# Performance work log

Hardware: AMD Instinct MI355X
Metric: run time of the kernel (lower is better)

## Reference

```python
import jax, jax.numpy as jnp
import numpy as np
import math

D_MODEL = 1024
NUM_HEADS = 16
D_K = D_MODEL // NUM_HEADS
MAX_SEQ_LEN = 2048
ROPE_THETA = 10000.0
BATCH = 4
SEQ = 2048


def _rope_buffers():
    inv_freq = 1.0 / (ROPE_THETA ** (jnp.arange(0, D_K, 2, dtype=jnp.float32) / D_K))
    positions = jnp.arange(MAX_SEQ_LEN, dtype=jnp.float32)
    angles = jnp.einsum('i,j->ij', positions, inv_freq)  # [max_seq_len, d_k/2]
    return jnp.cos(angles), jnp.sin(angles)


def setup_inputs() -> dict:
    key = jax.random.key(0)
    kx, kq, kk, kv, ko = jax.random.split(key, 5)
    std = math.sqrt(2.0 / (D_MODEL + D_MODEL))
    x = jax.random.normal(kx, (BATCH, SEQ, D_MODEL), dtype=jnp.float32)
    pos_ids = jnp.broadcast_to(jnp.arange(SEQ, dtype=jnp.int64), (BATCH, SEQ))
    Wq = jax.random.normal(kq, (D_MODEL, D_MODEL), dtype=jnp.float32) * std
    Wk = jax.random.normal(kk, (D_MODEL, D_MODEL), dtype=jnp.float32) * std
    Wv = jax.random.normal(kv, (D_MODEL, D_MODEL), dtype=jnp.float32) * std
    Wo = jax.random.normal(ko, (D_MODEL, D_MODEL), dtype=jnp.float32) * std
    cos, sin = _rope_buffers()
    return {"x": x, "pos_ids": pos_ids, "Wq": Wq, "Wk": Wk, "Wv": Wv, "Wo": Wo, "cos": cos, "sin": sin}


def _apply_rope(t, pos_ids, cos, sin):
    # t: [B, H, S, D_K]; interleaved (even, odd) pair rotation, as in the torch module
    cp = cos[pos_ids][:, None, :, :]  # [B,1,S,D_K/2]
    sp = sin[pos_ids][:, None, :, :]
    tr = t.reshape(*t.shape[:-1], D_K // 2, 2)
    t0, t1 = tr[..., 0], tr[..., 1]
    rot = jnp.stack((t0 * cp - t1 * sp, t0 * sp + t1 * cp), axis=-1)
    return rot.reshape(t.shape)


def reference(x, pos_ids, Wq, Wk, Wv, Wo, cos, sin):
    B, S, _ = x.shape
    def proj(W):
        return jnp.matmul(x, W.T).reshape(B, S, NUM_HEADS, D_K).transpose(0, 2, 1, 3)
    Q = _apply_rope(proj(Wq), pos_ids, cos, sin)
    K = _apply_rope(proj(Wk), pos_ids, cos, sin)
    V = proj(Wv)
    scores = jnp.einsum('bhqd,bhkd->bhqk', Q, K) / math.sqrt(D_K)
    causal = jnp.tril(jnp.ones((S, S), dtype=bool))
    scores = jnp.where(causal, scores, -jnp.inf)
    attn = jax.nn.softmax(scores, axis=-1)
    out = jnp.einsum('bhqk,bhkd->bhqd', attn, V)
    out = out.transpose(0, 2, 1, 3).reshape(B, S, D_MODEL)
    return jnp.matmul(out, Wo.T)
```

## Files before the change

kernel.cpp:

```cpp
#include <hip/hip_runtime.h>
#include <hip/hip_bf16.h>

typedef __bf16 bf16;
typedef __bf16 bf16x4 __attribute__((ext_vector_type(4)));
typedef __bf16 bf16x8 __attribute__((ext_vector_type(8)));
typedef float f32x4 __attribute__((ext_vector_type(4)));
typedef unsigned int u32;

#define BATCH 4
#define SEQN 2048
#define NH 16
#define DK 64
#define DM 1024
#define MROWS (BATCH*SEQN)

__device__ __forceinline__ void async16(bf16* lds, const bf16* g) {
  __builtin_amdgcn_global_load_lds(
      (const __attribute__((address_space(1))) u32*)g,
      (__attribute__((address_space(3))) u32*)lds, 16, 0, 0);
}

__global__ void cvt_all_kernel(const float4* __restrict__ x,  const float4* __restrict__ wq,
                               const float4* __restrict__ wk, const float4* __restrict__ wv,
                               const float4* __restrict__ wo,
                               bf16x4* __restrict__ xb, bf16x4* __restrict__ wqkvb,
                               bf16x4* __restrict__ wob) {
  const int NX = MROWS*DM/4, NW = DM*DM/4;
  int i = blockIdx.x*256 + threadIdx.x;
  const float4* s; bf16x4* d; int j;
  if (i < NX)             { s = x;  d = xb;         j = i; }
  else if (i < NX+NW)     { s = wq; d = wqkvb;      j = i-NX; }
  else if (i < NX+2*NW)   { s = wk; d = wqkvb+NW;   j = i-NX-NW; }
  else if (i < NX+3*NW)   { s = wv; d = wqkvb+2*NW; j = i-NX-2*NW; }
  else if (i < NX+4*NW)   { s = wo; d = wob;        j = i-NX-3*NW; }
  else return;
  float4 f = s[j];
  bf16x4 v;
  v[0] = (bf16)f.x; v[1] = (bf16)f.y; v[2] = (bf16)f.z; v[3] = (bf16)f.w;
  d[j] = v;
}

__device__ __forceinline__ void stage_half(bf16* slot, const bf16* src) {
  const int tid = threadIdx.x; const int w = tid >> 6;
#pragma unroll
  for (int j = 0; j < 2; ++j) {
    int L = j*512 + tid;
    int row = L >> 3;
    int dc  = (L & 7) ^ (row & 7);
    async16(slot + (size_t)(j*512 + w*64)*8, src + (size_t)row*DM + dc*8);
  }
}

#define SBAR() do { __builtin_amdgcn_sched_barrier(0); \
                    __builtin_amdgcn_s_barrier();       \
                    __builtin_amdgcn_sched_barrier(0); } while(0)

#define GPHASE(Ab, Bb, Q, STAGE, FW)  do {                                       \
    bf16x8 afr[2][2];                                                            \
    _Pragma("unroll")                                                            \
    for (int m = 0; m < 2; ++m) {                                                \
      const int row = wm + ((2*(Q)+m)<<4) + lc;                                  \
      _Pragma("unroll")                                                          \
      for (int kk = 0; kk < 2; ++kk)                                             \
        afr[m][kk] = *(const bf16x8*)((Ab) + (size_t)((row<<3) + ((kk*4+quad) ^ (row&7)))*8); \
    }                                                                            \
    if ((Q) == 0) {                                                              \
      _Pragma("unroll")                                                          \
      for (int nt = 0; nt < 4; ++nt) {                                           \
        const int row = wn + (nt<<4) + lc;                                       \
        _Pragma("unroll")                                                        \
        for (int kk = 0; kk < 2; ++kk)                                           \
          bfr[nt][kk] = *(const bf16x8*)((Bb) + (size_t)((row<<3) + ((kk*4+quad) ^ (row&7)))*8); \
      }                                                                          \
    }                                                                            \
    STAGE;                                                                       \
    SBAR();                                                                      \
    asm volatile("s_waitcnt lgkmcnt(0)" ::: "memory");                           \
    __builtin_amdgcn_sched_barrier(0);                                           \
    __builtin_amdgcn_s_setprio(1);                                               \
    _Pragma("unroll")                                                            \
    for (int kk = 0; kk < 2; ++kk)                                               \
      _Pragma("unroll")                                                          \
      for (int m = 0; m < 2; ++m)                                                \
        _Pragma("unroll")                                                        \
        for (int nt = 0; nt < 4; ++nt)                                           \
          acc[2*(Q)+m][nt] = __builtin_amdgcn_mfma_f32_16x16x32_bf16(afr[m][kk], bfr[nt][kk], acc[2*(Q)+m][nt], 0, 0, 0); \
    __builtin_amdgcn_s_setprio(0);                                               \
    FW;                                                                          \
    SBAR();                                                                      \
  } while (0)

__device__ __forceinline__ void gemm_core256(const bf16* __restrict__ Ag,
    const bf16* __restrict__ Bg, int r0, int c0, bf16* sm, f32x4 (&acc)[8][4]) {
  const int tid  = threadIdx.x;
  const int lane = tid & 63, quad = lane >> 4, lc = lane & 15;
  const int w = tid >> 6;
  const int wm = (w >> 2)*128, wn = (w & 3)*64;
  const int NT = DM/64;
  bf16* As[2] = { sm,         sm + 16384 };
  bf16* Bs[2] = { sm + 32768, sm + 49152 };

  auto stA = [&](int t, int h) {
    int tt = t < NT ? t : NT-1;
    stage_half(As[t&1] + h*8192, Ag + (size_t)(r0 + h*128)*DM + tt*64);
  };
  auto stB = [&](int t, int h) {
    int tt = t < NT ? t : NT-1;
    stage_half(Bs[t&1] + h*8192, Bg + (size_t)(c0 + h*128)*DM + tt*64);
  };

  stA(0,0); stA(0,1); stB(0,0); stB(0,1);
  stB(1,0); stB(1,1);
  asm volatile("s_waitcnt vmcnt(4)" ::: "memory");
  SBAR();

  bf16x8 bfr[4][2];
  for (int X = 0; X < NT/2; ++X) {
    const int t0 = 2*X;
    GPHASE(As[0], Bs[0], 0, stA(t0+1,0), );
    GPHASE(As[0], Bs[0], 1, stA(t0+1,1), );
    GPHASE(As[0], Bs[0], 2, stB(t0+2,0), );
    GPHASE(As[0], Bs[0], 3, stB(t0+2,1), asm volatile("s_waitcnt vmcnt(4)" ::: "memory"));
    GPHASE(As[1], Bs[1], 0, stA(t0+2,0), );
    GPHASE(As[1], Bs[1], 1, stA(t0+2,1), );
    GPHASE(As[1], Bs[1], 2, stB(t0+3,0), );
    GPHASE(As[1], Bs[1], 3, stB(t0+3,1), asm volatile("s_waitcnt vmcnt(4)" ::: "memory"));
  }
}

#define VS 136
__global__ __launch_bounds__(512, 2) void gemm_qkv_kernel(const bf16* __restrict__ A,
    const bf16* __restrict__ Bt, const float* __restrict__ cosb, const float* __restrict__ sinb,
    bf16* __restrict__ Q, bf16* __restrict__ K, bf16* __restrict__ Vt) {
  __shared__ __align__(16) bf16 sm[65536];
  f32x4 acc[8][4] = {};
  const int r0 = blockIdx.y*256, c0 = blockIdx.x*256;
  gemm_core256(A, Bt, r0, c0, sm, acc);
  const int tid  = threadIdx.x;
  const int lane = tid & 63, quad = lane >> 4, lc = lane & 15;
  const int w = tid >> 6;
  const int wm = (w >> 2)*128, wn = (w & 3)*64;
  const int which = c0 >> 10;
  if (which < 2) {
    bf16* T = which == 0 ? Q : K;
#pragma unroll
    for (int mt = 0; mt < 8; ++mt)
#pragma unroll
      for (int r = 0; r < 4; ++r) {
        int gr = r0 + wm + mt*16 + quad*4 + r;
        int b = gr >> 11, s = gr & (SEQN-1);
#pragma unroll
        for (int nt = 0; nt < 4; ++nt) {
          int gc = c0 + wn + nt*16 + lc;
          int c = gc & (DM-1), h = c >> 6, d = c & 63, p = d >> 1;
          float cc = cosb[s*32 + p], ss = sinb[s*32 + p];
          float v  = acc[mt][nt][r];
          float ov = __shfl_xor(v, 1, 64);
          float outv = ((lc & 1) == 0) ? (v*cc - ov*ss) : (ov*ss + v*cc);
          T[(((size_t)(b*NH + h))*SEQN + s)*DK + d] = (bf16)outv;
        }
      }
  } else {
    asm volatile("s_waitcnt vmcnt(0)" ::: "memory");
    __builtin_amdgcn_sched_barrier(0);
    __syncthreads();
    const int b = r0 >> 11, s_base = r0 & (SEQN-1);
    const int h0 = (c0 & (DM-1)) >> 6;
#pragma unroll
    for (int p = 0; p < 2; ++p) {
      if ((w >> 2) == p) {
#pragma unroll
        for (int mt = 0; mt < 8; ++mt)
#pragma unroll
          for (int nt = 0; nt < 4; ++nt) {
            int col = wn + nt*16 + lc;
            bf16x4 vv;
#pragma unroll
            for (int r = 0; r < 4; ++r) vv[r] = (bf16)acc[mt][nt][r];
            *(bf16x4*)(sm + (size_t)col*VS + mt*16 + quad*4) = vv;
          }
      }
      __syncthreads();
#pragma unroll
      for (int it = 0; it < 8; ++it) {
        int dall = it*32 + (tid >> 4);
        int s_off = (tid & 15)*8;
        bf16x8 vv = *(const bf16x8*)(sm + (size_t)dall*VS + s_off);
        int h = h0 + (dall >> 6), d = dall & 63;
        *(bf16x8*)(Vt + (((size_t)(b*NH + h))*DK + d)*SEQN + s_base + p*128 + s_off) = vv;
      }
      __syncthreads();
    }
  }
}

__global__ __launch_bounds__(512, 2) void gemm_out_kernel(const bf16* __restrict__ A,
    const bf16* __restrict__ Bt, float* __restrict__ C) {
  __shared__ __align__(16) bf16 sm[65536];
  f32x4 acc[8][4] = {};
  const int r0 = blockIdx.y*256, c0 = blockIdx.x*256;
  gemm_core256(A, Bt, r0, c0, sm, acc);
  const int tid  = threadIdx.x;
  const int lane = tid & 63, quad = lane >> 4, lc = lane & 15;
  const int w = tid >> 6;
  const int wm = (w >> 2)*128, wn = (w & 3)*64;
#pragma unroll
  for (int mt = 0; mt < 8; ++mt)
#pragma unroll
    for (int nt = 0; nt < 4; ++nt)
#pragma unroll
      for (int r = 0; r < 4; ++r) {
        int gr = r0 + wm + mt*16 + quad*4 + r;
        int gc = c0 + wn + nt*16 + lc;
        C[(size_t)gr*DM + gc] = acc[mt][nt][r];
      }
}

__global__ __launch_bounds__(256, 3) void attn_kernel(const bf16* __restrict__ Q,
    const bf16* __restrict__ K, const bf16* __restrict__ Vt, bf16* __restrict__ Oa) {
  __shared__ __align__(16) bf16 Ks[2][64*64];
  __shared__ __align__(16) bf16 Vs[2][64*64];
  __shared__ __align__(16) bf16 Pw[4][32*72];
  const int tid  = threadIdx.x;
  const int w = tid >> 6, lane = tid & 63;
  const int quad = lane >> 4, lc = lane & 15;
  const int bh = blockIdx.x;
  const int qt = (SEQN/128 - 1) - blockIdx.y;
  const int q0 = qt*128;
  const int qr0 = q0 + w*32;
  const bf16* Qp = Q  + (size_t)bh*SEQN*DK;
  const bf16* Kp = K  + (size_t)bh*SEQN*DK;
  const bf16* Vp = Vt + (size_t)bh*DK*SEQN;
  const float SC = 0.125f * 1.44269504f;
  bf16x8 aq[2][2];
#pragma unroll
  for (int mt = 0; mt < 2; ++mt)
#pragma unroll
    for (int kk = 0; kk < 2; ++kk) {
      bf16x8 raw = *(const bf16x8*)(Qp + (size_t)(qr0 + mt*16 + lc)*DK + kk*32 + quad*8);
#pragma unroll
      for (int j = 0; j < 8; ++j) raw[j] = (bf16)((float)raw[j] * SC);
      aq[mt][kk] = raw;
    }
  f32x4 o[2][4] = {};
  float lrow[2][4] = {};
  bf16* P = Pw[w];
  const int nsteps = 2*(qt + 1);

  auto stage = [&](int kt, int buf) {
#pragma unroll
    for (int j = 0; j < 2; ++j) {
      int L = j*256 + w*64 + lane;
      int row = L >> 3;
      int s8  = (L & 7) ^ (row & 7);
      bf16* kb = &Ks[buf][(size_t)(j*256 + w*64)*8];
      async16(kb, Kp + (size_t)(kt*64 + row)*DK + s8*8);
      bf16* vb = &Vs[buf][(size_t)(j*256 + w*64)*8];
      async16(vb, Vp + (size_t)row*SEQN + kt*64 + s8*8);
    }
  };

  stage(0, 0);
  for (int kt = 0; kt < nsteps; ++kt) {
    const int k0 = kt*64;
    const int cbuf = kt & 1;
    __syncthreads();
    if (kt + 1 < nsteps) stage(kt + 1, cbuf ^ 1);
    if (k0 <= qr0 + 31) {
      const bf16* Kt = Ks[cbuf];
      const bf16* Vc = Vs[cbuf];
      const int lastkey = qr0 + 31;
      f32x4 st[2][4] = {};
#pragma unroll
      for (int kk = 0; kk < 2; ++kk) {
        const int dc = kk*4 + quad;
        bf16x8 bk[4];
#pragma unroll
        for (int nt = 0; nt < 4; ++nt) {
          if (k0 + nt*16 <= lastkey) {
            int kr = nt*16 + lc;
            bk[nt] = *(const bf16x8*)(Kt + (size_t)(kr*8 + (dc ^ (kr & 7)))*8);
          }
        }
#pragma unroll
        for (int nt = 0; nt < 4; ++nt) {
          if (k0 + nt*16 <= lastkey) {
#pragma unroll
            for (int mt = 0; mt < 2; ++mt)
              st[mt][nt] = __builtin_amdgcn_mfma_f32_16x16x32_bf16(aq[mt][kk], bk[nt], st[mt][nt], 0, 0, 0);
          }
        }
      }
#pragma unroll
      for (int mt = 0; mt < 2; ++mt) {
        const int rmin = qr0 + mt*16, rmax = rmin + 15;
#pragma unroll
        for (int nt = 0; nt < 4; ++nt) {
          const int kmin = k0 + nt*16, kmax = kmin + 15;
          f32x4 p;
          if (kmax <= rmin) {
#pragma unroll
            for (int r = 0; r < 4; ++r) p[r] = exp2f(st[mt][nt][r]);
          } else if (kmin > rmax) {
            p = f32x4{0.f, 0.f, 0.f, 0.f};
          } else {
            const int key = kmin + lc;
#pragma unroll
            for (int r = 0; r < 4; ++r) {
              float v = exp2f(st[mt][nt][r]);
              p[r] = (key > rmin + quad*4 + r) ? 0.f : v;
            }
          }
          st[mt][nt] = p;
#pragma unroll
          for (int r = 0; r < 4; ++r) lrow[mt][r] += p[r];
        }
      }
#pragma unroll
      for (int mt = 0; mt < 2; ++mt)
#pragma unroll
        for (int r = 0; r < 4; ++r)
#pragma unroll
          for (int nt = 0; nt < 4; ++nt)
            P[(mt*16 + quad*4 + r)*72 + nt*16 + lc] = (bf16)st[mt][nt][r];
      asm volatile("s_waitcnt lgkmcnt(0)" ::: "memory");
#pragma unroll
      for (int kk = 0; kk < 2; ++kk) {
        if (k0 + kk*32 <= lastkey) {
          bf16x8 ap[2];
#pragma unroll
          for (int mt = 0; mt < 2; ++mt)
            ap[mt] = *(const bf16x8*)(P + (mt*16 + lc)*72 + kk*32 + quad*8);
          const int kc = kk*4 + quad;
          bf16x8 bv[4];
#pragma unroll
          for (int nb = 0; nb < 4; ++nb) {
            int dr = nb*16 + lc;
            bv[nb] = *(const bf16x8*)(Vc + (size_t)(dr*8 + (kc ^ (dr & 7)))*8);
          }
#pragma unroll
          for (int mt = 0; mt < 2; ++mt)
#pragma unroll
            for (int nb = 0; nb < 4; ++nb)
              o[mt][nb] = __builtin_amdgcn_mfma_f32_16x16x32_bf16(ap[mt], bv[nb], o[mt][nb], 0, 0, 0);
        }
      }
      asm volatile("s_waitcnt lgkmcnt(0)" ::: "memory");
    }
  }
#pragma unroll
  for (int off = 1; off < 16; off <<= 1)
#pragma unroll
    for (int mt = 0; mt < 2; ++mt)
#pragma unroll
      for (int r = 0; r < 4; ++r)
        lrow[mt][r] += __shfl_xor(lrow[mt][r], off, 64);
  const int b = bh >> 4, h = bh & 15;
#pragma unroll
  for (int mt = 0; mt < 2; ++mt)
#pragma unroll
    for (int r = 0; r < 4; ++r) {
      float inv = 1.f / lrow[mt][r];
      int qrow = qr0 + mt*16 + quad*4 + r;
      size_t rowoff = ((size_t)b*SEQN + qrow)*DM + h*DK;
#pragma unroll
      for (int nb = 0; nb < 4; ++nb)
        Oa[rowoff + nb*16 + lc] = (bf16)(o[mt][nb][r]*inv);
    }
}

extern "C" void kernel_launch(void* const* d_in, const int* in_sizes, int n_in,
                              void* d_out, int out_size, void* d_ws, size_t ws_size,
                              hipStream_t stream) {
  const float* x    = (const float*)d_in[0];
  const float* Wq   = (const float*)d_in[2];
  const float* Wk   = (const float*)d_in[3];
  const float* Wv   = (const float*)d_in[4];
  const float* Wo   = (const float*)d_in[5];
  const float* cosb = (const float*)d_in[6];
  const float* sinb = (const float*)d_in[7];
  float* out = (float*)d_out;

  char* ws = (char*)d_ws;
  const size_t SZ_X  = (size_t)MROWS*DM*2;
  const size_t SZ_W  = (size_t)DM*DM*2;
  bf16* xb   = (bf16*)(ws);
  bf16* wqkv = (bf16*)(ws + SZ_X);
  bf16* wo_b = (bf16*)(ws + SZ_X + 3*SZ_W);
  bf16* Qb   = (bf16*)(ws + SZ_X + 4*SZ_W);
  bf16* Kb   = (bf16*)(ws + 2*SZ_X + 4*SZ_W);
  bf16* Vtb  = (bf16*)(ws + 3*SZ_X + 4*SZ_W);
  bf16* Oa   = (bf16*)(ws + 4*SZ_X + 4*SZ_W);

  {
    const int NX = MROWS*DM/4, NW = DM*DM/4;
    int nblk = (NX + 4*NW + 255)/256;
    cvt_all_kernel<<<nblk, 256, 0, stream>>>((const float4*)x, (const float4*)Wq,
        (const float4*)Wk, (const float4*)Wv, (const float4*)Wo,
        (bf16x4*)xb, (bf16x4*)wqkv, (bf16x4*)wo_b);
  }
  gemm_qkv_kernel<<<dim3(3*DM/256, MROWS/256), 512, 0, stream>>>(xb, wqkv, cosb, sinb, Qb, Kb, Vtb);
  attn_kernel<<<dim3(BATCH*NH, SEQN/128), 256, 0, stream>>>(Qb, Kb, Vtb, Oa);
  gemm_out_kernel<<<dim3(DM/256, MROWS/256), 512, 0, stream>>>(Oa, wo_b, out);
}
```

Measured before the change: 268.4 us.

## Shrink GEMM tiles to 128x256 and use native exp2 in attention

```diff
diff --git a/kernel.cpp b/kernel.cpp
--- a/kernel.cpp
+++ b/kernel.cpp
@@ -90,26 +90,26 @@
     SBAR();                                                                      \
   } while (0)
 
-__device__ __forceinline__ void gemm_core256(const bf16* __restrict__ Ag,
-    const bf16* __restrict__ Bg, int r0, int c0, bf16* sm, f32x4 (&acc)[8][4]) {
+__device__ __forceinline__ void gemm_core128x256(const bf16* __restrict__ Ag,
+    const bf16* __restrict__ Bg, int r0, int c0, bf16* sm, f32x4 (&acc)[4][4]) {
   const int tid  = threadIdx.x;
   const int lane = tid & 63, quad = lane >> 4, lc = lane & 15;
   const int w = tid >> 6;
-  const int wm = (w >> 2)*128, wn = (w & 3)*64;
+  const int wm = (w >> 2)*64, wn = (w & 3)*64;
   const int NT = DM/64;
-  bf16* As[2] = { sm,         sm + 16384 };
-  bf16* Bs[2] = { sm + 32768, sm + 49152 };
-
-  auto stA = [&](int t, int h) {
+  bf16* As_[2] = { sm,         sm + 8192  };
+  bf16* Bs_[2] = { sm + 16384, sm + 32768 };
+
+  auto stA = [&](int t) {
     int tt = t < NT ? t : NT-1;
-    stage_half(As[t&1] + h*8192, Ag + (size_t)(r0 + h*128)*DM + tt*64);
+    stage_half(As_[t&1], Ag + (size_t)r0*DM + tt*64);
   };
   auto stB = [&](int t, int h) {
     int tt = t < NT ? t : NT-1;
-    stage_half(Bs[t&1] + h*8192, Bg + (size_t)(c0 + h*128)*DM + tt*64);
+    stage_half(Bs_[t&1] + h*8192, Bg + (size_t)(c0 + h*128)*DM + tt*64);
   };
 
-  stA(0,0); stA(0,1); stB(0,0); stB(0,1);
+  stB(0,0); stB(0,1); stA(0);
   stB(1,0); stB(1,1);
   asm volatile("s_waitcnt vmcnt(4)" ::: "memory");
   SBAR();
@@ -117,14 +117,10 @@
   bf16x8 bfr[4][2];
   for (int X = 0; X < NT/2; ++X) {
     const int t0 = 2*X;
-    GPHASE(As[0], Bs[0], 0, stA(t0+1,0), );
-    GPHASE(As[0], Bs[0], 1, stA(t0+1,1), );
-    GPHASE(As[0], Bs[0], 2, stB(t0+2,0), );
-    GPHASE(As[0], Bs[0], 3, stB(t0+2,1), asm volatile("s_waitcnt vmcnt(4)" ::: "memory"));
-    GPHASE(As[1], Bs[1], 0, stA(t0+2,0), );
-    GPHASE(As[1], Bs[1], 1, stA(t0+2,1), );
-    GPHASE(As[1], Bs[1], 2, stB(t0+3,0), );
-    GPHASE(As[1], Bs[1], 3, stB(t0+3,1), asm volatile("s_waitcnt vmcnt(4)" ::: "memory"));
+    GPHASE(As_[0], Bs_[0], 0, stA(t0+1), );
+    GPHASE(As_[0], Bs_[0], 1, stB(t0+2,0); stB(t0+2,1), asm volatile("s_waitcnt vmcnt(4)" ::: "memory"));
+    GPHASE(As_[1], Bs_[1], 0, stA(t0+2), );
+    GPHASE(As_[1], Bs_[1], 1, stB(t0+3,0); stB(t0+3,1), asm volatile("s_waitcnt vmcnt(4)" ::: "memory"));
   }
 }
 
@@ -132,19 +128,19 @@
 __global__ __launch_bounds__(512, 2) void gemm_qkv_kernel(const bf16* __restrict__ A,
     const bf16* __restrict__ Bt, const float* __restrict__ cosb, const float* __restrict__ sinb,
     bf16* __restrict__ Q, bf16* __restrict__ K, bf16* __restrict__ Vt) {
-  __shared__ __align__(16) bf16 sm[65536];
-  f32x4 acc[8][4] = {};
-  const int r0 = blockIdx.y*256, c0 = blockIdx.x*256;
-  gemm_core256(A, Bt, r0, c0, sm, acc);
+  __shared__ __align__(16) bf16 sm[49152];
+  f32x4 acc[4][4] = {};
+  const int r0 = blockIdx.y*128, c0 = blockIdx.x*256;
+  gemm_core128x256(A, Bt, r0, c0, sm, acc);
   const int tid  = threadIdx.x;
   const int lane = tid & 63, quad = lane >> 4, lc = lane & 15;
   const int w = tid >> 6;
-  const int wm = (w >> 2)*128, wn = (w & 3)*64;
+  const int wm = (w >> 2)*64, wn = (w & 3)*64;
   const int which = c0 >> 10;
   if (which < 2) {
     bf16* T = which == 0 ? Q : K;
 #pragma unroll
-    for (int mt = 0; mt < 8; ++mt)
+    for (int mt = 0; mt < 4; ++mt)
 #pragma unroll
       for (int r = 0; r < 4; ++r) {
         int gr = r0 + wm + mt*16 + quad*4 + r;
@@ -164,48 +160,42 @@
     asm volatile("s_waitcnt vmcnt(0)" ::: "memory");
     __builtin_amdgcn_sched_barrier(0);
     __syncthreads();
+#pragma unroll
+    for (int mt = 0; mt < 4; ++mt)
+#pragma unroll
+      for (int nt = 0; nt < 4; ++nt) {
+        int col = wn + nt*16 + lc;
+        bf16x4 vv;
+#pragma unroll
+        for (int r = 0; r < 4; ++r) vv[r] = (bf16)acc[mt][nt][r];
+        *(bf16x4*)(sm + (size_t)col*VS + wm + mt*16 + quad*4) = vv;
+      }
+    __syncthreads();
     const int b = r0 >> 11, s_base = r0 & (SEQN-1);
     const int h0 = (c0 & (DM-1)) >> 6;
 #pragma unroll
-    for (int p = 0; p < 2; ++p) {
-      if ((w >> 2) == p) {
-#pragma unroll
-        for (int mt = 0; mt < 8; ++mt)
-#pragma unroll
-          for (int nt = 0; nt < 4; ++nt) {
-            int col = wn + nt*16 + lc;
-            bf16x4 vv;
-#pragma unroll
-            for (int r = 0; r < 4; ++r) vv[r] = (bf16)acc[mt][nt][r];
-            *(bf16x4*)(sm + (size_t)col*VS + mt*16 + quad*4) = vv;
-          }
-      }
-      __syncthreads();
-#pragma unroll
-      for (int it = 0; it < 8; ++it) {
-        int dall = it*32 + (tid >> 4);
-        int s_off = (tid & 15)*8;
-        bf16x8 vv = *(const bf16x8*)(sm + (size_t)dall*VS + s_off);
-        int h = h0 + (dall >> 6), d = dall & 63;
-        *(bf16x8*)(Vt + (((size_t)(b*NH + h))*DK + d)*SEQN + s_base + p*128 + s_off) = vv;
-      }
-      __syncthreads();
+    for (int it = 0; it < 8; ++it) {
+      int dall = it*32 + (tid >> 4);
+      int s_off = (tid & 15)*8;
+      bf16x8 vv = *(const bf16x8*)(sm + (size_t)dall*VS + s_off);
+      int h = h0 + (dall >> 6), d = dall & 63;
+      *(bf16x8*)(Vt + (((size_t)(b*NH + h))*DK + d)*SEQN + s_base + s_off) = vv;
     }
   }
 }
 
 __global__ __launch_bounds__(512, 2) void gemm_out_kernel(const bf16* __restrict__ A,
     const bf16* __restrict__ Bt, float* __restrict__ C) {
-  __shared__ __align__(16) bf16 sm[65536];
-  f32x4 acc[8][4] = {};
-  const int r0 = blockIdx.y*256, c0 = blockIdx.x*256;
-  gemm_core256(A, Bt, r0, c0, sm, acc);
+  __shared__ __align__(16) bf16 sm[49152];
+  f32x4 acc[4][4] = {};
+  const int r0 = blockIdx.y*128, c0 = blockIdx.x*256;
+  gemm_core128x256(A, Bt, r0, c0, sm, acc);
   const int tid  = threadIdx.x;
   const int lane = tid & 63, quad = lane >> 4, lc = lane & 15;
   const int w = tid >> 6;
-  const int wm = (w >> 2)*128, wn = (w & 3)*64;
-#pragma unroll
-  for (int mt = 0; mt < 8; ++mt)
+  const int wm = (w >> 2)*64, wn = (w & 3)*64;
+#pragma unroll
+  for (int mt = 0; mt < 4; ++mt)
 #pragma unroll
     for (int nt = 0; nt < 4; ++nt)
 #pragma unroll
@@ -300,14 +290,14 @@
           f32x4 p;
           if (kmax <= rmin) {
 #pragma unroll
-            for (int r = 0; r < 4; ++r) p[r] = exp2f(st[mt][nt][r]);
+            for (int r = 0; r < 4; ++r) p[r] = __builtin_amdgcn_exp2f(st[mt][nt][r]);
           } else if (kmin > rmax) {
             p = f32x4{0.f, 0.f, 0.f, 0.f};
           } else {
             const int key = kmin + lc;
 #pragma unroll
             for (int r = 0; r < 4; ++r) {
-              float v = exp2f(st[mt][nt][r]);
+              float v = __builtin_amdgcn_exp2f(st[mt][nt][r]);
               p[r] = (key > rmin + quad*4 + r) ? 0.f : v;
             }
           }
@@ -399,7 +389,7 @@
         (const float4*)Wk, (const float4*)Wv, (const float4*)Wo,
         (bf16x4*)xb, (bf16x4*)wqkv, (bf16x4*)wo_b);
   }
-  gemm_qkv_kernel<<<dim3(3*DM/256, MROWS/256), 512, 0, stream>>>(xb, wqkv, cosb, sinb, Qb, Kb, Vtb);
+  gemm_qkv_kernel<<<dim3(3*DM/256, MROWS/128), 512, 0, stream>>>(xb, wqkv, cosb, sinb, Qb, Kb, Vtb);
   attn_kernel<<<dim3(BATCH*NH, SEQN/128), 256, 0, stream>>>(Qb, Kb, Vtb, Oa);
-  gemm_out_kernel<<<dim3(DM/256, MROWS/256), 512, 0, stream>>>(Oa, wo_b, out);
-}
+  gemm_out_kernel<<<dim3(DM/256, MROWS/128), 512, 0, stream>>>(Oa, wo_b, out);
+}
```

Result: faster. 249.0 us (-7.3%).
